# Performance work log

Measured on AMD Instinct MI355X. Metric: run time of the kernel, lower is better.

Reference implementation:

```python
import jax, jax.numpy as jnp
import numpy as np

H = 2            # attention heads
HID = 128        # hidden_channels
NEG_SLOPE = 0.2  # GATConv leaky_relu slope

N_USER, N_POST, N_ENT = 100000, 50000, 20000
TEXT_D, USER_D, ENT_D = 768, 64, 64
E_PUB, E_REP, E_CON, E_INT, E_FOL = 150000, 300000, 200000, 500000, 500000


def _gat(h_src, h_dst, src, dst, Wsrc, Wdst, asrc, adst, bias):
    """PyG GATConv((-1,-1), C, heads=H, concat=False, add_self_loops=False)."""
    n_dst = h_dst.shape[0]
    C = Wsrc.shape[1] // H
    xs = (h_src @ Wsrc).reshape(-1, H, C)          # [Ns,H,C]
    xd = (h_dst @ Wdst).reshape(-1, H, C)          # [Nd,H,C]
    al_s = jnp.einsum('nhc,hc->nh', xs, asrc)      # [Ns,H]
    al_d = jnp.einsum('nhc,hc->nh', xd, adst)      # [Nd,H]
    e = jax.nn.leaky_relu(al_s[src] + al_d[dst], NEG_SLOPE)   # [E,H]
    m = jax.ops.segment_max(e, dst, num_segments=n_dst)
    m = jnp.where(jnp.isfinite(m), m, 0.0)
    ex = jnp.exp(e - m[dst])
    denom = jax.ops.segment_sum(ex, dst, num_segments=n_dst)
    alpha = ex / (denom[dst] + 1e-16)              # per-dst softmax
    msg = xs[src] * alpha[:, :, None]              # [E,H,C]
    out = jax.ops.segment_sum(msg, dst, num_segments=n_dst)   # [Nd,H,C]
    return out.mean(axis=1) + bias                 # concat=False -> head mean


def setup_inputs() -> dict:
    key = jax.random.key(0)
    ks = jax.random.split(key, 24)
    s = 0.05
    d = {
        'post_cls': jax.random.normal(ks[0], (N_POST, TEXT_D), jnp.float32),
        'user_x': jax.random.normal(ks[1], (N_USER, USER_D), jnp.float32),
        'entity_x': jax.random.normal(ks[2], (N_ENT, ENT_D), jnp.float32),
        'Wpost': jax.random.normal(ks[3], (TEXT_D, HID), jnp.float32) * s,
        'bpost': jnp.zeros((HID,), jnp.float32),
        'Wuser': jax.random.normal(ks[4], (USER_D, HID), jnp.float32) * s,
        'buser': jnp.zeros((HID,), jnp.float32),
        'Went': jax.random.normal(ks[5], (ENT_D, HID), jnp.float32) * s,
        'bent': jnp.zeros((HID,), jnp.float32),
        # 2 layers x 5 relations (publish, repost, contain, interact, follow)
        'gat_Wsrc': jax.random.normal(ks[6], (2, 5, HID, H * HID), jnp.float32) * s,
        'gat_Wdst': jax.random.normal(ks[7], (2, 5, HID, H * HID), jnp.float32) * s,
        'gat_asrc': jax.random.normal(ks[8], (2, 5, H, HID), jnp.float32) * s,
        'gat_adst': jax.random.normal(ks[9], (2, 5, H, HID), jnp.float32) * s,
        'gat_bias': jnp.zeros((2, 5, HID), jnp.float32),
        'Wc1': jax.random.normal(ks[10], (HID, HID // 2), jnp.float32) * s,
        'bc1': jnp.zeros((HID // 2,), jnp.float32),
        'Wc2': jax.random.normal(ks[11], (HID // 2, 1), jnp.float32) * s,
        'bc2': jnp.zeros((1,), jnp.float32),
        'pub_src': jax.random.randint(ks[12], (E_PUB,), 0, N_USER, jnp.int32),
        'pub_dst': jax.random.randint(ks[13], (E_PUB,), 0, N_POST, jnp.int32),
        'rep_src': jax.random.randint(ks[14], (E_REP,), 0, N_USER, jnp.int32),
        'rep_dst': jax.random.randint(ks[15], (E_REP,), 0, N_POST, jnp.int32),
        'con_src': jax.random.randint(ks[16], (E_CON,), 0, N_POST, jnp.int32),
        'con_dst': jax.random.randint(ks[17], (E_CON,), 0, N_ENT, jnp.int32),
        'int_src': jax.random.randint(ks[18], (E_INT,), 0, N_USER, jnp.int32),
        'int_dst': jax.random.randint(ks[19], (E_INT,), 0, N_USER, jnp.int32),
        'fol_src': jax.random.randint(ks[20], (E_FOL,), 0, N_USER, jnp.int32),
        'fol_dst': jax.random.randint(ks[21], (E_FOL,), 0, N_USER, jnp.int32),
    }
    return d


def _forward(post_cls, user_x, entity_x, Wpost, bpost, Wuser, buser, Went, bent,
             gat_Wsrc, gat_Wdst, gat_asrc, gat_adst, gat_bias,
             Wc1, bc1, Wc2, bc2, edges):
    h = {
        'post': post_cls @ Wpost + bpost,
        'user': user_x @ Wuser + buser,
        'entity': entity_x @ Went + bent,
    }
    for l in range(2):
        def g(r, h_src, h_dst, src, dst):
            return _gat(h_src, h_dst, src, dst,
                        gat_Wsrc[l, r], gat_Wdst[l, r],
                        gat_asrc[l, r], gat_adst[l, r], gat_bias[l, r])
        # HeteroConv aggr='sum' over edge types sharing a dst node type
        new_post = (g(0, h['user'], h['post'], edges['pub_src'], edges['pub_dst'])
                    + g(1, h['user'], h['post'], edges['rep_src'], edges['rep_dst']))
        new_ent = g(2, h['post'], h['entity'], edges['con_src'], edges['con_dst'])
        new_user = (g(3, h['user'], h['user'], edges['int_src'], edges['int_dst'])
                    + g(4, h['user'], h['user'], edges['fol_src'], edges['fol_dst']))
        h = {'post': jax.nn.relu(new_post),
             'user': jax.nn.relu(new_user),
             'entity': jax.nn.relu(new_ent)}
    # classifier (dropout inactive at inference)
    z = jax.nn.relu(h['post'] @ Wc1 + bc1)
    out = z @ Wc2 + bc2
    return out.squeeze(-1)   # [n_posts]


def reference(post_cls, user_x, entity_x, Wpost, bpost, Wuser, buser, Went, bent,
              gat_Wsrc, gat_Wdst, gat_asrc, gat_adst, gat_bias,
              Wc1, bc1, Wc2, bc2,
              pub_src, pub_dst, rep_src, rep_dst, con_src, con_dst,
              int_src, int_dst, fol_src, fol_dst):
    edges = dict(pub_src=pub_src, pub_dst=pub_dst, rep_src=rep_src, rep_dst=rep_dst,
                 con_src=con_src, con_dst=con_dst, int_src=int_src, int_dst=int_dst,
                 fol_src=fol_src, fol_dst=fol_dst)
    return _forward(post_cls, user_x, entity_x, Wpost, bpost, Wuser, buser, Went, bent,
                    gat_Wsrc, gat_Wdst, gat_asrc, gat_adst, gat_bias,
                    Wc1, bc1, Wc2, bc2, edges)
```

## Files before the change

kernel.cpp:

```cpp
#include <hip/hip_runtime.h>
#include <cstdint>
#include <cstddef>

#define N_USER 100000
#define N_POST 50000
#define TEXT_D 768
#define USER_D 64
#define E_TOT 1450000
#define N_TOT 300000

typedef unsigned short ushort_t;
typedef float f4v __attribute__((ext_vector_type(4)));
typedef short s8v __attribute__((ext_vector_type(8)));
typedef unsigned short u4v __attribute__((ext_vector_type(4)));
typedef unsigned short u8v __attribute__((ext_vector_type(8)));

__device__ __forceinline__ float leaky(float v) { return v > 0.f ? v : 0.2f * v; }
__device__ __forceinline__ void split_bf(float x, ushort_t& hi, ushort_t& lo) {
  unsigned u = __float_as_uint(x);
  hi = (ushort_t)(u >> 16);
  float r = x - __uint_as_float(u & 0xFFFF0000u);
  lo = (ushort_t)(__float_as_uint(r) >> 16);
}

struct Ptrs4 { const int* p[4]; };

__global__ void wvec_kernel(const float* __restrict__ W, const float* __restrict__ av,
                            float* __restrict__ wv) {
  int b = blockIdx.x;
  int lr = b / 2, h = b % 2;
  const float* Wp = W + ((size_t)lr * 128 * 256) + (size_t)threadIdx.x * 256 + h * 128;
  const float* ap = av + (size_t)(lr * 2 + h) * 128;
  float acc = 0.f;
  for (int c = 0; c < 128; ++c) acc += Wp[c] * ap[c];
  wv[(size_t)(lr * 2 + h) * 128 + threadIdx.x] = acc;
}

__global__ void wt_prep(const float* __restrict__ W, ushort_t* __restrict__ WTh,
                        ushort_t* __restrict__ WTl, int K, int C) {
  int k = blockIdx.x * 256 + threadIdx.x;
  int c = blockIdx.y;
  if (k >= K) return;
  ushort_t h, l;
  split_bf(W[(size_t)k * C + c], h, l);
  WTh[(size_t)c * K + k] = h;
  WTl[(size_t)c * K + k] = l;
}

__global__ void stk_prep(const float* __restrict__ Wa, const float* __restrict__ Wb,
                         ushort_t* __restrict__ STh, ushort_t* __restrict__ STl) {
  int rel = blockIdx.x;
  int c = blockIdx.y;
  int t = threadIdx.x;
  const float* W = rel ? Wb : Wa;
  float v = W[(size_t)(t & 127) * 256 + (size_t)(t >> 7) * 128 + c];
  ushort_t hh, ll;
  split_bf(v, hh, ll);
  size_t idx = (size_t)c * 512 + (size_t)rel * 256 + t;
  STh[idx] = hh;
  STl[idx] = ll;
}

__global__ void bias_sum(const float* __restrict__ gbias, float* __restrict__ BS) {
  int c = threadIdx.x;
  BS[c]       = gbias[0 * 640 + 0 * 128 + c] + gbias[0 * 640 + 1 * 128 + c];
  BS[128 + c] = gbias[0 * 640 + 3 * 128 + c] + gbias[0 * 640 + 4 * 128 + c];
  BS[256 + c] = gbias[1 * 640 + 0 * 128 + c] + gbias[1 * 640 + 1 * 128 + c];
}

__global__ __launch_bounds__(512) void gemm_bregs(const float* __restrict__ Xf,
                                                  const ushort_t* __restrict__ Bgh,
                                                  const ushort_t* __restrict__ Bgl,
                                                  const float* __restrict__ bv,
                                                  float* __restrict__ Out,
                                                  int N, int K) {
  __shared__ ushort_t LAh[64 * 72], LAl[64 * 72];
  int t = threadIdx.x;
  int lane = t & 63, w = t >> 6;
  int m = lane & 15, quad = lane >> 4;
  int row0 = blockIdx.x * 64;
  int nkc = K >> 6;

  int sr = t >> 3, sk = (t & 7) * 8;
  int srow = row0 + sr; if (srow >= N) srow = N - 1;
  size_t abase = (size_t)srow * K + sk;
  size_t bb = (size_t)(w * 16 + m) * K;

  f4v acc[4];
#pragma unroll
  for (int mt = 0; mt < 4; ++mt) acc[mt] = (f4v){0.f, 0.f, 0.f, 0.f};

  float4 pf0, pf1;
  auto LOADA = [&](int kc) {
    size_t off = abase + (size_t)kc * 64;
    pf0 = *(const float4*)(Xf + off);
    pf1 = *(const float4*)(Xf + off + 4);
  };
  auto WRITEA = [&]() {
    u8v hh, ll;
    ushort_t h_, l_;
    split_bf(pf0.x, h_, l_); hh[0] = h_; ll[0] = l_;
    split_bf(pf0.y, h_, l_); hh[1] = h_; ll[1] = l_;
    split_bf(pf0.z, h_, l_); hh[2] = h_; ll[2] = l_;
    split_bf(pf0.w, h_, l_); hh[3] = h_; ll[3] = l_;
    split_bf(pf1.x, h_, l_); hh[4] = h_; ll[4] = l_;
    split_bf(pf1.y, h_, l_); hh[5] = h_; ll[5] = l_;
    split_bf(pf1.z, h_, l_); hh[6] = h_; ll[6] = l_;
    split_bf(pf1.w, h_, l_); hh[7] = h_; ll[7] = l_;
    *(u8v*)&LAh[sr * 72 + sk] = hh;
    *(u8v*)&LAl[sr * 72 + sk] = ll;
  };

  LOADA(0);
  for (int kc = 0; kc < nkc; ++kc) {
    WRITEA();
    __syncthreads();
    if (kc + 1 < nkc) LOADA(kc + 1);
    size_t bo = bb + (size_t)kc * 64 + quad * 8;
    s8v bh0 = *(const s8v*)(Bgh + bo);
    s8v bl0 = *(const s8v*)(Bgl + bo);
    s8v bh1 = *(const s8v*)(Bgh + bo + 32);
    s8v bl1 = *(const s8v*)(Bgl + bo + 32);
#pragma unroll
    for (int mt = 0; mt < 4; ++mt) {
      int ar = (mt * 16 + m) * 72 + quad * 8;
      s8v ah = *(const s8v*)&LAh[ar];
      s8v al = *(const s8v*)&LAl[ar];
      acc[mt] = __builtin_amdgcn_mfma_f32_16x16x32_bf16(ah, bh0, acc[mt], 0, 0, 0);
      acc[mt] = __builtin_amdgcn_mfma_f32_16x16x32_bf16(ah, bl0, acc[mt], 0, 0, 0);
      acc[mt] = __builtin_amdgcn_mfma_f32_16x16x32_bf16(al, bh0, acc[mt], 0, 0, 0);
    }
#pragma unroll
    for (int mt = 0; mt < 4; ++mt) {
      int ar = (mt * 16 + m) * 72 + 32 + quad * 8;
      s8v ah = *(const s8v*)&LAh[ar];
      s8v al = *(const s8v*)&LAl[ar];
      acc[mt] = __builtin_amdgcn_mfma_f32_16x16x32_bf16(ah, bh1, acc[mt], 0, 0, 0);
      acc[mt] = __builtin_amdgcn_mfma_f32_16x16x32_bf16(ah, bl1, acc[mt], 0, 0, 0);
      acc[mt] = __builtin_amdgcn_mfma_f32_16x16x32_bf16(al, bh1, acc[mt], 0, 0, 0);
    }
    __syncthreads();
  }

  float bbv = bv[w * 16 + m];
#pragma unroll
  for (int mt = 0; mt < 4; ++mt)
#pragma unroll
    for (int j = 0; j < 4; ++j) {
      int row = row0 + mt * 16 + quad * 4 + j;
      if (row < N) Out[(size_t)row * 128 + w * 16 + m] = acc[mt][j] + bbv;
    }
}

__device__ __forceinline__ void rel_of(int g, int& r, int& loc, int& nb) {
  if (g < 450000) {
    if (g < 150000) { r = 0; loc = g;          nb = 0; }
    else            { r = 1; loc = g - 150000; nb = 50000; }
  } else if (g < 950000)  { r = 2; loc = g - 450000;  nb = 100000; }
  else                    { r = 3; loc = g - 950000;  nb = 200000; }
}
__global__ void histc_kernel(Ptrs4 dsts, int* __restrict__ cnt) {
  int g = blockIdx.x * 256 + threadIdx.x;
  if (g >= E_TOT) return;
  int r, loc, nb;
  rel_of(g, r, loc, nb);
  atomicAdd(&cnt[nb + dsts.p[r][loc]], 1);
}
__global__ __launch_bounds__(256) void scan1_kernel(const int* __restrict__ cnt,
                                                    int* __restrict__ excl,
                                                    int* __restrict__ partials, int Nd) {
  __shared__ int sb[256];
  int t = threadIdx.x;
  int base = blockIdx.x * 1024 + t * 4;
  int v[4];
#pragma unroll
  for (int j = 0; j < 4; ++j) v[j] = (base + j < Nd) ? cnt[base + j] : 0;
  int tot = v[0] + v[1] + v[2] + v[3];
  sb[t] = tot;
  __syncthreads();
  for (int off = 1; off < 256; off <<= 1) {
    int x = 0;
    if (t >= off) x = sb[t - off];
    __syncthreads();
    sb[t] += x;
    __syncthreads();
  }
  int ex = sb[t] - tot;
  if (t == 255) partials[blockIdx.x] = sb[t];
  int run = ex;
#pragma unroll
  for (int j = 0; j < 4; ++j) {
    if (base + j < Nd) excl[base + j] = run;
    run += v[j];
  }
}
__global__ __launch_bounds__(512) void scan2_kernel(int* __restrict__ partials, int B) {
  __shared__ int sb[512];
  int t = threadIdx.x;
  int v = (t < B) ? partials[t] : 0;
  sb[t] = v;
  __syncthreads();
  for (int off = 1; off < 512; off <<= 1) {
    int x = 0;
    if (t >= off) x = sb[t - off];
    __syncthreads();
    sb[t] += x;
    __syncthreads();
  }
  if (t < B) partials[t] = sb[t] - v;
}
__global__ void scan3_kernel(const int* __restrict__ excl, const int* __restrict__ partials,
                             int* __restrict__ rowptr, int* __restrict__ cursor) {
  int i = blockIdx.x * 256 + threadIdx.x;
  if (i < N_TOT) {
    int v = excl[i] + partials[i >> 10];
    rowptr[i] = v;
    cursor[i] = v;
  }
  if (i == 0) rowptr[N_TOT] = E_TOT;
}
__global__ void scatterc_kernel(Ptrs4 srcs, Ptrs4 dsts,
                                int* __restrict__ cursor, int* __restrict__ csrc) {
  int g = blockIdx.x * 256 + threadIdx.x;
  if (g >= E_TOT) return;
  int r, loc, nb;
  rel_of(g, r, loc, nb);
  int p = atomicAdd(&cursor[nb + dsts.p[r][loc]], 1);
  csrc[p] = srcs.p[r][loc];
}

__global__ __launch_bounds__(256) void logits2_kernel(const float* __restrict__ H,
                                                      const float* __restrict__ wsA,
                                                      const float* __restrict__ wsB,
                                                      float* __restrict__ alsA,
                                                      float* __restrict__ alsB, int Ns) {
  int n = blockIdx.x * 4 + (threadIdx.x >> 6);
  int lane = threadIdx.x & 63;
  if (n >= Ns) return;
  const float* hr = H + (size_t)n * 128;
  float ha = hr[lane], hb = hr[lane + 64];
  float p0 = ha * wsA[lane] + hb * wsA[lane + 64];
  float p1 = ha * wsA[128 + lane] + hb * wsA[192 + lane];
  float p2 = ha * wsB[lane] + hb * wsB[lane + 64];
  float p3 = ha * wsB[128 + lane] + hb * wsB[192 + lane];
#pragma unroll
  for (int mk = 32; mk; mk >>= 1) {
    p0 += __shfl_xor(p0, mk); p1 += __shfl_xor(p1, mk);
    p2 += __shfl_xor(p2, mk); p3 += __shfl_xor(p3, mk);
  }
  if (lane == 0) {
    *(float2*)(alsA + 2 * (size_t)n) = make_float2(p0, p1);
    *(float2*)(alsB + 2 * (size_t)n) = make_float2(p2, p3);
  }
}

__global__ __launch_bounds__(256) void fusedagg_kernel(const int* __restrict__ rowA,
                                                       const int* __restrict__ rowB,
                                                       const int* __restrict__ csrc,
                                                       const float* __restrict__ alsA,
                                                       const float* __restrict__ alsB,
                                                       const float* __restrict__ wdvA,
                                                       const float* __restrict__ wdvB,
                                                       const float* __restrict__ Hs,
                                                       const float* __restrict__ Hd,
                                                       const ushort_t* __restrict__ Bgh,
                                                       const ushort_t* __restrict__ Bgl,
                                                       const float* __restrict__ bsv,
                                                       float* __restrict__ Out, int Nd) {
  __shared__ ushort_t LGh[16 * 544], LGl[16 * 544];
  int t = threadIdx.x;
  int hw = t >> 5;
  int s = t & 31;
  int d0 = blockIdx.x * 16;

#pragma unroll 1
  for (int i = 0; i < 4; ++i) {
    int tid = hw * 4 + i;
    int dl = tid >> 1, rel = tid & 1;
    int d = d0 + dl;
    const int* rp = rel ? rowB : rowA;
    const float* als = rel ? alsB : alsA;
    const float* wdv = rel ? wdvB : wdvA;

    const float* hr = Hd + (size_t)d * 128;
    float t0 = 0.f, t1 = 0.f;
#pragma unroll
    for (int j = 0; j < 4; ++j) {
      float hv = hr[s + 32 * j];
      t0 += hv * wdv[s + 32 * j];
      t1 += hv * wdv[128 + s + 32 * j];
    }
#pragma unroll
    for (int mk = 16; mk; mk >>= 1) { t0 += __shfl_xor(t0, mk); t1 += __shfl_xor(t1, mk); }

    int start = rp[d], end = rp[d + 1];
    float den0 = 0.f, den1 = 0.f;
    f4v a0 = (f4v){0.f, 0.f, 0.f, 0.f}, a1 = (f4v){0.f, 0.f, 0.f, 0.f};
    if (end > start) {
      int last = end - 1;
      for (int b0 = start; b0 < end; b0 += 8) {
        int sid[8]; bool vl[8];
#pragma unroll
        for (int j = 0; j < 8; ++j) {
          int ee = b0 + j;
          vl[j] = ee < end;
          sid[j] = csrc[vl[j] ? ee : last];
        }
        float2 al2[8]; f4v x[8];
#pragma unroll
        for (int j = 0; j < 8; ++j) {
          al2[j] = *(const float2*)(als + 2 * (size_t)sid[j]);
          x[j] = *(const f4v*)(Hs + (size_t)sid[j] * 128 + 4 * s);
        }
#pragma unroll
        for (int j = 0; j < 8; ++j) {
          float w0 = vl[j] ? __expf(leaky(al2[j].x + t0)) : 0.f;
          float w1 = vl[j] ? __expf(leaky(al2[j].y + t1)) : 0.f;
          den0 += w0; den1 += w1;
#pragma unroll
          for (int q = 0; q < 4; ++q) { a0[q] += w0 * x[j][q]; a1[q] += w1 * x[j][q]; }
        }
      }
    }
    float i0 = 0.5f / (den0 + 1e-16f);
    float i1 = 0.5f / (den1 + 1e-16f);
    int base = dl * 544 + rel * 256;
    u4v g0h, g0l, g1h, g1l;
#pragma unroll
    for (int q = 0; q < 4; ++q) {
      ushort_t hh, ll;
      split_bf(a0[q] * i0, hh, ll); g0h[q] = hh; g0l[q] = ll;
      split_bf(a1[q] * i1, hh, ll); g1h[q] = hh; g1l[q] = ll;
    }
    *(u4v*)&LGh[base + 4 * s] = g0h;
    *(u4v*)&LGl[base + 4 * s] = g0l;
    *(u4v*)&LGh[base + 128 + 4 * s] = g1h;
    *(u4v*)&LGl[base + 128 + 4 * s] = g1l;
  }
  __syncthreads();

  int lane = t & 63, w = t >> 6;
  int m = lane & 15, quad = lane >> 4;
  f4v acc0 = (f4v){0.f, 0.f, 0.f, 0.f};
  f4v acc1 = (f4v){0.f, 0.f, 0.f, 0.f};
  size_t cb0 = (size_t)(w * 32 + m) * 512;
  size_t cb1 = (size_t)(w * 32 + 16 + m) * 512;
#pragma unroll
  for (int kc = 0; kc < 16; ++kc) {
    int ko = kc * 32 + quad * 8;
    s8v ah = *(const s8v*)&LGh[m * 544 + ko];
    s8v al = *(const s8v*)&LGl[m * 544 + ko];
    s8v b0h = *(const s8v*)(Bgh + cb0 + ko);
    s8v b0l = *(const s8v*)(Bgl + cb0 + ko);
    s8v b1h = *(const s8v*)(Bgh + cb1 + ko);
    s8v b1l = *(const s8v*)(Bgl + cb1 + ko);
    acc0 = __builtin_amdgcn_mfma_f32_16x16x32_bf16(ah, b0h, acc0, 0, 0, 0);
    acc0 = __builtin_amdgcn_mfma_f32_16x16x32_bf16(ah, b0l, acc0, 0, 0, 0);
    acc0 = __builtin_amdgcn_mfma_f32_16x16x32_bf16(al, b0h, acc0, 0, 0, 0);
    acc1 = __builtin_amdgcn_mfma_f32_16x16x32_bf16(ah, b1h, acc1, 0, 0, 0);
    acc1 = __builtin_amdgcn_mfma_f32_16x16x32_bf16(ah, b1l, acc1, 0, 0, 0);
    acc1 = __builtin_amdgcn_mfma_f32_16x16x32_bf16(al, b1h, acc1, 0, 0, 0);
  }
  float bb0 = bsv[w * 32 + m], bb1 = bsv[w * 32 + 16 + m];
#pragma unroll
  for (int j = 0; j < 4; ++j) {
    int row = d0 + quad * 4 + j;
    float* o = Out + (size_t)row * 128 + w * 32;
    o[m] = fmaxf(acc0[j] + bb0, 0.f);
    o[16 + m] = fmaxf(acc1[j] + bb1, 0.f);
  }
}

__global__ __launch_bounds__(256) void classifier_kernel(const float* __restrict__ Hp,
                                                         const float* __restrict__ Wc1, const float* __restrict__ bc1,
                                                         const float* __restrict__ Wc2, const float* __restrict__ bc2,
                                                         float* __restrict__ out, int N) {
  __shared__ float sW[128 * 64];
  int t = threadIdx.x;
#pragma unroll
  for (int i = 0; i < 8; ++i) ((float4*)sW)[t + 256 * i] = ((const float4*)Wc1)[t + 256 * i];
  __syncthreads();
  int lane = t & 63, wv = t >> 6;
  float b = bc1[lane], w2 = Wc2[lane], b2 = bc2[0];
#pragma unroll
  for (int nn = 0; nn < 2; ++nn) {
    int n = blockIdx.x * 8 + wv * 2 + nn;
    if (n >= N) continue;
    const float* hr = Hp + (size_t)n * 128;
    float accz = b;
    for (int k = 0; k < 128; ++k) accz += hr[k] * sW[k * 64 + lane];
    float z = fmaxf(accz, 0.f) * w2;
#pragma unroll
    for (int off = 32; off; off >>= 1) z += __shfl_down(z, off);
    if (lane == 0) out[n] = z + b2;
  }
}

extern "C" void kernel_launch(void* const* d_in, const int* in_sizes, int n_in,
                              void* d_out, int out_size, void* d_ws, size_t ws_size,
                              hipStream_t stream) {
  const float* post_cls = (const float*)d_in[0];
  const float* user_x   = (const float*)d_in[1];
  const float* Wpost = (const float*)d_in[3];
  const float* bpost = (const float*)d_in[4];
  const float* Wuser = (const float*)d_in[5];
  const float* buser = (const float*)d_in[6];
  const float* gWsrc = (const float*)d_in[9];
  const float* gWdst = (const float*)d_in[10];
  const float* gasrc = (const float*)d_in[11];
  const float* gadst = (const float*)d_in[12];
  const float* gbias = (const float*)d_in[13];
  const float* Wc1 = (const float*)d_in[14];
  const float* bc1 = (const float*)d_in[15];
  const float* Wc2 = (const float*)d_in[16];
  const float* bc2 = (const float*)d_in[17];
  Ptrs4 SRCS, DSTS;
  SRCS.p[0] = (const int*)d_in[18]; DSTS.p[0] = (const int*)d_in[19];
  SRCS.p[1] = (const int*)d_in[20]; DSTS.p[1] = (const int*)d_in[21];
  SRCS.p[2] = (const int*)d_in[24]; DSTS.p[2] = (const int*)d_in[25];
  SRCS.p[3] = (const int*)d_in[26]; DSTS.p[3] = (const int*)d_in[27];
  float* out = (float*)d_out;
  (void)ws_size; (void)in_sizes; (void)n_in; (void)out_size;

  float* Wf = (float*)d_ws;
  size_t o = 0;
  float* WDSTV = Wf + o; o += 2560;
  float* WSRCV = Wf + o; o += 2560;
  float* BS    = Wf + o; o += 384;
  float* ALSa  = Wf + o; o += (size_t)N_USER * 2;
  float* ALSb  = Wf + o; o += (size_t)N_USER * 2;
  float* HU    = Wf + o; o += (size_t)N_USER * 128;
  float* HU2   = Wf + o; o += (size_t)N_USER * 128;
  float* HP    = Wf + o; o += (size_t)N_POST * 128;
  int* Wi = (int*)(Wf + o);
  size_t io = 0;
  int* RP   = Wi + io; io += N_TOT + 1;
  int* CURS = Wi + io; io += N_TOT;
  int* CNT  = Wi + io; io += N_TOT;
  int* EXCL = Wi + io; io += N_TOT;
  int* PART = Wi + io; io += 512;
  int* CSRC = Wi + io; io += E_TOT;
  io = (io + 7) & ~(size_t)7;
  ushort_t* Wu = (ushort_t*)(Wi + io);
  size_t uo = 0;
  ushort_t* PWh = Wu + uo; uo += 128 * TEXT_D;
  ushort_t* PWl = Wu + uo; uo += 128 * TEXT_D;
  ushort_t* UWh = Wu + uo; uo += 128 * USER_D;
  ushort_t* UWl = Wu + uo; uo += 128 * USER_D;
  ushort_t* STh[3]; ushort_t* STl[3];
  for (int i = 0; i < 3; ++i) {
    STh[i] = Wu + uo; uo += 128 * 512;
    STl[i] = Wu + uo; uo += 128 * 512;
  }

  const int NOFF_PUB = 0, NOFF_REP = 50000, NOFF_INT = 100000, NOFF_FOL = 200000;

  (void)hipMemsetAsync(CNT, 0, (size_t)N_TOT * sizeof(int), stream);
  histc_kernel<<<(E_TOT + 255) / 256, 256, 0, stream>>>(DSTS, CNT);
  int B = (N_TOT + 1023) / 1024;
  scan1_kernel<<<B, 256, 0, stream>>>(CNT, EXCL, PART, N_TOT);
  scan2_kernel<<<1, 512, 0, stream>>>(PART, B);
  scan3_kernel<<<(N_TOT + 255) / 256, 256, 0, stream>>>(EXCL, PART, RP, CURS);
  scatterc_kernel<<<(E_TOT + 255) / 256, 256, 0, stream>>>(SRCS, DSTS, CURS, CSRC);

  wt_prep<<<dim3(3, 128), 256, 0, stream>>>(Wpost, PWh, PWl, TEXT_D, 128);
  wt_prep<<<dim3(1, 128), 256, 0, stream>>>(Wuser, UWh, UWl, USER_D, 128);
  stk_prep<<<dim3(2, 128), 256, 0, stream>>>(gWsrc + (size_t)0 * 32768, gWsrc + (size_t)1 * 32768, STh[0], STl[0]);
  stk_prep<<<dim3(2, 128), 256, 0, stream>>>(gWsrc + (size_t)3 * 32768, gWsrc + (size_t)4 * 32768, STh[1], STl[1]);
  stk_prep<<<dim3(2, 128), 256, 0, stream>>>(gWsrc + (size_t)5 * 32768, gWsrc + (size_t)6 * 32768, STh[2], STl[2]);
  wvec_kernel<<<20, 128, 0, stream>>>(gWdst, gadst, WDSTV);
  wvec_kernel<<<20, 128, 0, stream>>>(gWsrc, gasrc, WSRCV);
  bias_sum<<<1, 128, 0, stream>>>(gbias, BS);

  gemm_bregs<<<(N_POST + 63) / 64, 512, 0, stream>>>(
      post_cls, PWh, PWl, bpost, HP, N_POST, TEXT_D);
  gemm_bregs<<<(N_USER + 63) / 64, 512, 0, stream>>>(
      user_x, UWh, UWl, buser, HU, N_USER, USER_D);

  logits2_kernel<<<(N_USER + 3) / 4, 256, 0, stream>>>(
      HU, WSRCV + 0 * 256, WSRCV + 1 * 256, ALSa, ALSb, N_USER);
  fusedagg_kernel<<<N_POST / 16, 256, 0, stream>>>(
      RP + NOFF_PUB, RP + NOFF_REP, CSRC, ALSa, ALSb,
      WDSTV + 0 * 256, WDSTV + 1 * 256, HU, HP,
      STh[0], STl[0], BS + 0, HP, N_POST);

  logits2_kernel<<<(N_USER + 3) / 4, 256, 0, stream>>>(
      HU, WSRCV + 3 * 256, WSRCV + 4 * 256, ALSa, ALSb, N_USER);
  fusedagg_kernel<<<N_USER / 16, 256, 0, stream>>>(
      RP + NOFF_INT, RP + NOFF_FOL, CSRC, ALSa, ALSb,
      WDSTV + 3 * 256, WDSTV + 4 * 256, HU, HU,
      STh[1], STl[1], BS + 128, HU2, N_USER);

  logits2_kernel<<<(N_USER + 3) / 4, 256, 0, stream>>>(
      HU2, WSRCV + 5 * 256, WSRCV + 6 * 256, ALSa, ALSb, N_USER);
  fusedagg_kernel<<<N_POST / 16, 256, 0, stream>>>(
      RP + NOFF_PUB, RP + NOFF_REP, CSRC, ALSa, ALSb,
      WDSTV + 5 * 256, WDSTV + 6 * 256, HU2, HP,
      STh[2], STl[2], BS + 256, HP, N_POST);

  classifier_kernel<<<(N_POST + 7) / 8, 256, 0, stream>>>(HP, Wc1, bc1, Wc2, bc2, out, N_POST);
}
```

Measured before the change: 1.203 ms.

## Double fused aggregation block to 512 threads, one half-wave per destination

The fused GAT aggregation kernel now runs 512 threads per block. Each 32-lane half-wave owns one destination node and loops over both relations, instead of each half-wave looping over four (dst, relation) tasks. The MFMA epilogue spreads the 128 output columns over 8 waves of 16 columns each, cutting per-wave MFMA work and register use. It also shrinks the LDS row padding and adds bounds guards. The aim is more parallelism on the gather phase, at the cost of a larger block and possible occupancy or LDS bank-conflict changes.

```diff
diff --git a/kernel.cpp b/kernel.cpp
--- a/kernel.cpp
+++ b/kernel.cpp
@@ -254,7 +254,7 @@
   }
 }
 
-__global__ __launch_bounds__(256) void fusedagg_kernel(const int* __restrict__ rowA,
+__global__ __launch_bounds__(512) void fusedagg_kernel(const int* __restrict__ rowA,
                                                        const int* __restrict__ rowB,
                                                        const int* __restrict__ csrc,
                                                        const float* __restrict__ alsA,
@@ -267,107 +267,105 @@
                                                        const ushort_t* __restrict__ Bgl,
                                                        const float* __restrict__ bsv,
                                                        float* __restrict__ Out, int Nd) {
-  __shared__ ushort_t LGh[16 * 544], LGl[16 * 544];
+  __shared__ ushort_t LGh[16 * 520], LGl[16 * 520];
   int t = threadIdx.x;
   int hw = t >> 5;
   int s = t & 31;
   int d0 = blockIdx.x * 16;
 
-#pragma unroll 1
-  for (int i = 0; i < 4; ++i) {
-    int tid = hw * 4 + i;
-    int dl = tid >> 1, rel = tid & 1;
-    int d = d0 + dl;
-    const int* rp = rel ? rowB : rowA;
-    const float* als = rel ? alsB : alsA;
-    const float* wdv = rel ? wdvB : wdvA;
-
+  {
+    int dl = hw;
+    int d = d0 + dl; if (d >= Nd) d = Nd - 1;
     const float* hr = Hd + (size_t)d * 128;
-    float t0 = 0.f, t1 = 0.f;
+    float t0A = 0.f, t1A = 0.f, t0B = 0.f, t1B = 0.f;
 #pragma unroll
     for (int j = 0; j < 4; ++j) {
       float hv = hr[s + 32 * j];
-      t0 += hv * wdv[s + 32 * j];
-      t1 += hv * wdv[128 + s + 32 * j];
+      t0A += hv * wdvA[s + 32 * j];
+      t1A += hv * wdvA[128 + s + 32 * j];
+      t0B += hv * wdvB[s + 32 * j];
+      t1B += hv * wdvB[128 + s + 32 * j];
     }
 #pragma unroll
-    for (int mk = 16; mk; mk >>= 1) { t0 += __shfl_xor(t0, mk); t1 += __shfl_xor(t1, mk); }
-
-    int start = rp[d], end = rp[d + 1];
-    float den0 = 0.f, den1 = 0.f;
-    f4v a0 = (f4v){0.f, 0.f, 0.f, 0.f}, a1 = (f4v){0.f, 0.f, 0.f, 0.f};
-    if (end > start) {
-      int last = end - 1;
-      for (int b0 = start; b0 < end; b0 += 8) {
-        int sid[8]; bool vl[8];
-#pragma unroll
-        for (int j = 0; j < 8; ++j) {
-          int ee = b0 + j;
-          vl[j] = ee < end;
-          sid[j] = csrc[vl[j] ? ee : last];
-        }
-        float2 al2[8]; f4v x[8];
-#pragma unroll
-        for (int j = 0; j < 8; ++j) {
-          al2[j] = *(const float2*)(als + 2 * (size_t)sid[j]);
-          x[j] = *(const f4v*)(Hs + (size_t)sid[j] * 128 + 4 * s);
-        }
-#pragma unroll
-        for (int j = 0; j < 8; ++j) {
-          float w0 = vl[j] ? __expf(leaky(al2[j].x + t0)) : 0.f;
-          float w1 = vl[j] ? __expf(leaky(al2[j].y + t1)) : 0.f;
-          den0 += w0; den1 += w1;
-#pragma unroll
-          for (int q = 0; q < 4; ++q) { a0[q] += w0 * x[j][q]; a1[q] += w1 * x[j][q]; }
+    for (int mk = 16; mk; mk >>= 1) {
+      t0A += __shfl_xor(t0A, mk); t1A += __shfl_xor(t1A, mk);
+      t0B += __shfl_xor(t0B, mk); t1B += __shfl_xor(t1B, mk);
+    }
+
+#pragma unroll 1
+    for (int rel = 0; rel < 2; ++rel) {
+      const int* rp = rel ? rowB : rowA;
+      const float* als = rel ? alsB : alsA;
+      float t0 = rel ? t0B : t0A;
+      float t1 = rel ? t1B : t1A;
+
+      int start = rp[d], end = rp[d + 1];
+      float den0 = 0.f, den1 = 0.f;
+      f4v a0 = (f4v){0.f, 0.f, 0.f, 0.f}, a1 = (f4v){0.f, 0.f, 0.f, 0.f};
+      if (end > start) {
+        int last = end - 1;
+        for (int b0 = start; b0 < end; b0 += 8) {
+          int sid[8]; bool vl[8];
+#pragma unroll
+          for (int j = 0; j < 8; ++j) {
+            int ee = b0 + j;
+            vl[j] = ee < end;
+            sid[j] = csrc[vl[j] ? ee : last];
+          }
+          float2 al2[8]; f4v x[8];
+#pragma unroll
+          for (int j = 0; j < 8; ++j) {
+            al2[j] = *(const float2*)(als + 2 * (size_t)sid[j]);
+            x[j] = *(const f4v*)(Hs + (size_t)sid[j] * 128 + 4 * s);
+          }
+#pragma unroll
+          for (int j = 0; j < 8; ++j) {
+            float w0 = vl[j] ? __expf(leaky(al2[j].x + t0)) : 0.f;
+            float w1 = vl[j] ? __expf(leaky(al2[j].y + t1)) : 0.f;
+            den0 += w0; den1 += w1;
+#pragma unroll
+            for (int q = 0; q < 4; ++q) { a0[q] += w0 * x[j][q]; a1[q] += w1 * x[j][q]; }
+          }
         }
       }
+      float i0 = 0.5f / (den0 + 1e-16f);
+      float i1 = 0.5f / (den1 + 1e-16f);
+      int base = dl * 520 + rel * 256;
+      u4v g0h, g0l, g1h, g1l;
+#pragma unroll
+      for (int q = 0; q < 4; ++q) {
+        ushort_t hh, ll;
+        split_bf(a0[q] * i0, hh, ll); g0h[q] = hh; g0l[q] = ll;
+        split_bf(a1[q] * i1, hh, ll); g1h[q] = hh; g1l[q] = ll;
+      }
+      *(u4v*)&LGh[base + 4 * s] = g0h;
+      *(u4v*)&LGl[base + 4 * s] = g0l;
+      *(u4v*)&LGh[base + 128 + 4 * s] = g1h;
+      *(u4v*)&LGl[base + 128 + 4 * s] = g1l;
     }
-    float i0 = 0.5f / (den0 + 1e-16f);
-    float i1 = 0.5f / (den1 + 1e-16f);
-    int base = dl * 544 + rel * 256;
-    u4v g0h, g0l, g1h, g1l;
-#pragma unroll
-    for (int q = 0; q < 4; ++q) {
-      ushort_t hh, ll;
-      split_bf(a0[q] * i0, hh, ll); g0h[q] = hh; g0l[q] = ll;
-      split_bf(a1[q] * i1, hh, ll); g1h[q] = hh; g1l[q] = ll;
-    }
-    *(u4v*)&LGh[base + 4 * s] = g0h;
-    *(u4v*)&LGl[base + 4 * s] = g0l;
-    *(u4v*)&LGh[base + 128 + 4 * s] = g1h;
-    *(u4v*)&LGl[base + 128 + 4 * s] = g1l;
   }
   __syncthreads();
 
   int lane = t & 63, w = t >> 6;
   int m = lane & 15, quad = lane >> 4;
-  f4v acc0 = (f4v){0.f, 0.f, 0.f, 0.f};
-  f4v acc1 = (f4v){0.f, 0.f, 0.f, 0.f};
-  size_t cb0 = (size_t)(w * 32 + m) * 512;
-  size_t cb1 = (size_t)(w * 32 + 16 + m) * 512;
+  f4v acc = (f4v){0.f, 0.f, 0.f, 0.f};
+  size_t cb = (size_t)(w * 16 + m) * 512;
 #pragma unroll
   for (int kc = 0; kc < 16; ++kc) {
     int ko = kc * 32 + quad * 8;
-    s8v ah = *(const s8v*)&LGh[m * 544 + ko];
-    s8v al = *(const s8v*)&LGl[m * 544 + ko];
-    s8v b0h = *(const s8v*)(Bgh + cb0 + ko);
-    s8v b0l = *(const s8v*)(Bgl + cb0 + ko);
-    s8v b1h = *(const s8v*)(Bgh + cb1 + ko);
-    s8v b1l = *(const s8v*)(Bgl + cb1 + ko);
-    acc0 = __builtin_amdgcn_mfma_f32_16x16x32_bf16(ah, b0h, acc0, 0, 0, 0);
-    acc0 = __builtin_amdgcn_mfma_f32_16x16x32_bf16(ah, b0l, acc0, 0, 0, 0);
-    acc0 = __builtin_amdgcn_mfma_f32_16x16x32_bf16(al, b0h, acc0, 0, 0, 0);
-    acc1 = __builtin_amdgcn_mfma_f32_16x16x32_bf16(ah, b1h, acc1, 0, 0, 0);
-    acc1 = __builtin_amdgcn_mfma_f32_16x16x32_bf16(ah, b1l, acc1, 0, 0, 0);
-    acc1 = __builtin_amdgcn_mfma_f32_16x16x32_bf16(al, b1h, acc1, 0, 0, 0);
-  }
-  float bb0 = bsv[w * 32 + m], bb1 = bsv[w * 32 + 16 + m];
+    s8v ah = *(const s8v*)&LGh[m * 520 + ko];
+    s8v al = *(const s8v*)&LGl[m * 520 + ko];
+    s8v bh = *(const s8v*)(Bgh + cb + ko);
+    s8v bl = *(const s8v*)(Bgl + cb + ko);
+    acc = __builtin_amdgcn_mfma_f32_16x16x32_bf16(ah, bh, acc, 0, 0, 0);
+    acc = __builtin_amdgcn_mfma_f32_16x16x32_bf16(ah, bl, acc, 0, 0, 0);
+    acc = __builtin_amdgcn_mfma_f32_16x16x32_bf16(al, bh, acc, 0, 0, 0);
+  }
+  float bb = bsv[w * 16 + m];
 #pragma unroll
   for (int j = 0; j < 4; ++j) {
     int row = d0 + quad * 4 + j;
-    float* o = Out + (size_t)row * 128 + w * 32;
-    o[m] = fmaxf(acc0[j] + bb0, 0.f);
-    o[16 + m] = fmaxf(acc1[j] + bb1, 0.f);
+    if (row < Nd) Out[(size_t)row * 128 + w * 16 + m] = fmaxf(acc[j] + bb, 0.f);
   }
 }
 
@@ -479,21 +477,21 @@
 
   logits2_kernel<<<(N_USER + 3) / 4, 256, 0, stream>>>(
       HU, WSRCV + 0 * 256, WSRCV + 1 * 256, ALSa, ALSb, N_USER);
-  fusedagg_kernel<<<N_POST / 16, 256, 0, stream>>>(
+  fusedagg_kernel<<<(N_POST + 15) / 16, 512, 0, stream>>>(
       RP + NOFF_PUB, RP + NOFF_REP, CSRC, ALSa, ALSb,
       WDSTV + 0 * 256, WDSTV + 1 * 256, HU, HP,
       STh[0], STl[0], BS + 0, HP, N_POST);
 
   logits2_kernel<<<(N_USER + 3) / 4, 256, 0, stream>>>(
       HU, WSRCV + 3 * 256, WSRCV + 4 * 256, ALSa, ALSb, N_USER);
-  fusedagg_kernel<<<N_USER / 16, 256, 0, stream>>>(
+  fusedagg_kernel<<<(N_USER + 15) / 16, 512, 0, stream>>>(
       RP + NOFF_INT, RP + NOFF_FOL, CSRC, ALSa, ALSb,
       WDSTV + 3 * 256, WDSTV + 4 * 256, HU, HU,
       STh[1], STl[1], BS + 128, HU2, N_USER);
 
   logits2_kernel<<<(N_USER + 3) / 4, 256, 0, stream>>>(
       HU2, WSRCV + 5 * 256, WSRCV + 6 * 256, ALSa, ALSb, N_USER);
-  fusedagg_kernel<<<N_POST / 16, 256, 0, stream>>>(
+  fusedagg_kernel<<<(N_POST + 15) / 16, 512, 0, stream>>>(
       RP + NOFF_PUB, RP + NOFF_REP, CSRC, ALSa, ALSb,
       WDSTV + 5 * 256, WDSTV + 6 * 256, HU2, HP,
       STh[2], STl[2], BS + 256, HP, N_POST);
```

After: 1.256 ms. 4.4% more time.
